# Optimization experiments

Hardware: AMD Instinct MI355X
Metric: run time of the kernel (lower is better)

Reference implementation:

```python
import jax, jax.numpy as jnp
import numpy as np
from jax import lax

DIM = 512
HEADS = 8
B, H, W = 8, 64, 64
EPS = 1e-12  # F.normalize default eps


def pointwise(x, w):
    # 1x1 conv, no bias: [B,C,H,W] x [O,C] -> [B,O,H,W]
    return jnp.einsum('oc,bchw->bohw', w, x)


def depthwise3x3(x, dw):
    # groups=C depthwise 3x3 conv, padding=1, no bias. dw: [C,1,3,3]
    return lax.conv_general_dilated(
        x, dw, window_strides=(1, 1), padding=((1, 1), (1, 1)),
        feature_group_count=x.shape[1],
        dimension_numbers=('NCHW', 'OIHW', 'NCHW'))


def setup_inputs() -> dict:
    key = jax.random.key(0)
    ks = jax.random.split(key, 8)
    s = 1.0 / np.sqrt(DIM)
    return {
        'x': jax.random.normal(ks[0], (B, DIM, H, W), jnp.float32),
        'w_q': jax.random.normal(ks[1], (DIM, DIM), jnp.float32) * s,
        'w_k': jax.random.normal(ks[2], (DIM, DIM), jnp.float32) * s,
        'w_v': jax.random.normal(ks[3], (DIM, DIM), jnp.float32) * s,
        'dw_q': jax.random.normal(ks[4], (DIM, 1, 3, 3), jnp.float32) * (1.0 / 3.0),
        'dw_k': jax.random.normal(ks[5], (DIM, 1, 3, 3), jnp.float32) * (1.0 / 3.0),
        'dw_v': jax.random.normal(ks[6], (DIM, 1, 3, 3), jnp.float32) * (1.0 / 3.0),
        'w_proj': jax.random.normal(ks[7], (DIM, DIM), jnp.float32) * s,
        'temperature': jnp.ones((HEADS, 1, 1), jnp.float32),
    }


def reference(x, w_q, w_k, w_v, dw_q, dw_k, dw_v, w_proj, temperature):
    b, c, h, w = x.shape
    d = c // HEADS
    hw = h * w

    q = depthwise3x3(pointwise(x, w_q), dw_q)
    k = depthwise3x3(pointwise(x, w_k), dw_k)
    v = depthwise3x3(pointwise(x, w_v), dw_v)

    # b (h d) x y -> b h d (x y)
    q = q.reshape(b, HEADS, d, hw)
    k = k.reshape(b, HEADS, d, hw)
    v = v.reshape(b, HEADS, d, hw)

    # L2-normalize over spatial axis (F.normalize, eps=1e-12)
    q = q / jnp.maximum(jnp.linalg.norm(q, axis=-1, keepdims=True), EPS)
    k = k / jnp.maximum(jnp.linalg.norm(k, axis=-1, keepdims=True), EPS)

    # channel attention: [b,h,d,d]
    attn = jnp.einsum('bhdn,bhen->bhde', q, k) * temperature
    attn = jax.nn.softmax(attn, axis=-1)
    out = jnp.einsum('bhde,bhen->bhdn', attn, v)  # [b,h,d,hw]

    out = out.reshape(b, c, h, w)
    return pointwise(out, w_proj)
```

## Files before the change

### kernel.cpp

```cpp
#include <hip/hip_runtime.h>
#include <hip/hip_bf16.h>
#include <stdint.h>

#define DEV __device__ __forceinline__

typedef __attribute__((ext_vector_type(8))) short   s16x8;
typedef __attribute__((ext_vector_type(8))) __bf16  bf16x8;
typedef __attribute__((ext_vector_type(4))) float   f32x4;

static constexpr int BATCH = 8;
static constexpr int DIM   = 512;
static constexpr int HEADS = 8;
static constexpr int HD    = 64;
static constexpr int HW    = 4096;
static constexpr int CQKV  = 1536;
static constexpr int NSPLIT = 8;

DEV void gload16(const void* g, void* l) {
  __builtin_amdgcn_global_load_lds(
      (const __attribute__((address_space(1))) void*)g,
      (__attribute__((address_space(3))) void*)l,
      16, 0, 0);
}

DEV f32x4 mfma16x32(s16x8 a, s16x8 b, f32x4 c) {
  return __builtin_amdgcn_mfma_f32_16x16x32_bf16(
      __builtin_bit_cast(bf16x8, a), __builtin_bit_cast(bf16x8, b), c, 0, 0, 0);
}

DEV float b2f(short x) {
  unsigned u = (unsigned)(unsigned short)x << 16;
  return __uint_as_float(u);
}
DEV short f2b(float f) { return __builtin_bit_cast(short, __float2bfloat16(f)); }

__global__ __launch_bounds__(256) void trx_prep(
    const float* __restrict__ x, __hip_bfloat16* __restrict__ XT,
    const float* __restrict__ wq, const float* __restrict__ wk,
    const float* __restrict__ wv, const float* __restrict__ wp,
    __hip_bfloat16* __restrict__ wqkv, __hip_bfloat16* __restrict__ wpb)
{
  const int t = threadIdx.x;
  if (blockIdx.z == 8) {
    long i0 = (((long)blockIdx.y * 64 + blockIdx.x) * 256 + t) * 8;
    const float* src;
    __hip_bfloat16* dst;
    long off;
    if (i0 < (long)CQKV * DIM) {
      int r = (int)(i0 >> 9);
      src = (r < 512) ? wq : (r < 1024) ? wk : wv;
      off = (long)(r & 511) * DIM + (i0 & 511);
      dst = wqkv + i0;
    } else {
      long j0 = i0 - (long)CQKV * DIM;
      src = wp; off = j0; dst = wpb + j0;
    }
    float4 a = *(const float4*)&src[off];
    float4 b = *(const float4*)&src[off + 4];
    s16x8 v;
    v[0] = f2b(a.x); v[1] = f2b(a.y); v[2] = f2b(a.z); v[3] = f2b(a.w);
    v[4] = f2b(b.x); v[5] = f2b(b.y); v[6] = f2b(b.z); v[7] = f2b(b.w);
    *(s16x8*)dst = v;
    return;
  }
  __shared__ float tile[64 * 65];
  const int n0 = blockIdx.x * 64, c0 = blockIdx.y * 64, b = blockIdx.z;
#pragma unroll
  for (int i = 0; i < 16; ++i) {
    int f = i * 256 + t; int ci = f >> 6, nj = f & 63;
    tile[ci * 65 + nj] = x[((long)b * DIM + c0 + ci) * HW + n0 + nj];
  }
  __syncthreads();
#pragma unroll
  for (int i = 0; i < 16; ++i) {
    int f = i * 256 + t; int ni = f >> 6, cj = f & 63;
    XT[((long)b * HW + n0 + ni) * DIM + c0 + cj] = __float2bfloat16(tile[cj * 65 + ni]);
  }
}

__global__ __launch_bounds__(512) void gemm_bt2(
    const __hip_bfloat16* __restrict__ A,
    const __hip_bfloat16* __restrict__ Bt,
    __hip_bfloat16* __restrict__ Cout,
    int M, int N, int K, long bt_bstride, long c_bstride)
{
  __shared__ __hip_bfloat16 lds[32768];
  const int t = threadIdx.x, w = t >> 6, l = t & 63;
  const int wm = w >> 2, wn = w & 3;
  const int m0 = blockIdx.y * 256, n0 = blockIdx.x * 256, b = blockIdx.z;
  const __hip_bfloat16* Bb = Bt + (long)b * bt_bstride;
  __hip_bfloat16* ldsA = lds;
  __hip_bfloat16* ldsB = lds + 16384;

  const int fr = l & 15, g = l >> 4;
  f32x4 acc[8][4] = {};

  for (int k0 = 0; k0 < K; k0 += 64) {
#pragma unroll
    for (int q = 0; q < 4; ++q) {
      int id = q * 512 + t;
      int r = id >> 3;
      int c = (id & 7) ^ (r & 7);
      gload16(A  + (long)(m0 + r) * K + k0 + c * 8, &ldsA[id * 8]);
      gload16(Bb + (long)(n0 + r) * K + k0 + c * 8, &ldsB[id * 8]);
    }
    __syncthreads();
#pragma unroll
    for (int kk = 0; kk < 64; kk += 32) {
      s16x8 af[8], bfr[4];
#pragma unroll
      for (int mi = 0; mi < 8; ++mi) {
        int ar = wm * 128 + mi * 16 + fr;
        int col = (kk + g * 8) ^ ((ar & 7) << 3);
        af[mi] = *(const s16x8*)&ldsA[ar * 64 + col];
      }
#pragma unroll
      for (int ni = 0; ni < 4; ++ni) {
        int br = wn * 64 + ni * 16 + fr;
        int col = (kk + g * 8) ^ ((br & 7) << 3);
        bfr[ni] = *(const s16x8*)&ldsB[br * 64 + col];
      }
#pragma unroll
      for (int mi = 0; mi < 8; ++mi)
#pragma unroll
        for (int ni = 0; ni < 4; ++ni)
          acc[mi][ni] = mfma16x32(af[mi], bfr[ni], acc[mi][ni]);
    }
    __syncthreads();
  }

  const int row0 = m0 + wm * 128, col0 = n0 + wn * 64;
#pragma unroll
  for (int mi = 0; mi < 8; ++mi)
#pragma unroll
    for (int ni = 0; ni < 4; ++ni)
#pragma unroll
      for (int j = 0; j < 4; ++j) {
        long rr = row0 + mi * 16 + (l >> 4) * 4 + j;
        long cc = col0 + ni * 16 + fr;
        Cout[(long)b * c_bstride + rr * N + cc] = __float2bfloat16(acc[mi][ni][j]);
      }
}

template <bool OUT_BF16>
__global__ __launch_bounds__(512, 2) void gemm_bt8(
    const __hip_bfloat16* __restrict__ A,
    const __hip_bfloat16* __restrict__ Bt,
    void* __restrict__ Cout,
    int M, int N, int K, long bt_bstride, long c_bstride)
{
  __shared__ __hip_bfloat16 lds[65536];
  const int t = threadIdx.x, w = t >> 6, l = t & 63;
  const int wm = w >> 2, wn = w & 3;
  const int m0 = blockIdx.y * 256, n0 = blockIdx.x * 256, b = blockIdx.z;
  const __hip_bfloat16* Bb = Bt + (long)b * bt_bstride;

  const int rl = t >> 3;
  const int ch = ((t & 7) ^ (rl & 7)) * 8;
  const int fr = l & 15, fk = (l >> 4) * 8;
  const int fswz = (l & 7) << 3;

  auto stageA = [&](int p, int h, int u) {
    const __hip_bfloat16* src = A + (long)(m0 + h * 64 + rl) * K + u * 64 + ch;
    __hip_bfloat16* dst = lds + p * 16384 + h * 8192 + w * 512;
    gload16(src, dst);
    gload16(src + 128l * K, dst + 4096);
  };
  auto stageB = [&](int p, int hb, int u) {
    const __hip_bfloat16* src = Bb + (long)(n0 + hb * 128 + rl) * K + u * 64 + ch;
    __hip_bfloat16* dst = lds + 32768 + p * 16384 + hb * 8192 + w * 512;
    gload16(src, dst);
    gload16(src + 64l * K, dst + 4096);
  };

  f32x4 acc[8][4] = {};
  const int NT = K >> 6;

  stageB(0, 0, 0); stageB(0, 1, 0); stageA(0, 0, 0); stageA(0, 1, 0);
  stageB(1, 0, 1); stageB(1, 1, 1); stageA(1, 0, 1);
  asm volatile("s_waitcnt vmcnt(6)" ::: "memory");
  __builtin_amdgcn_s_barrier();

  for (int u = 0; u < NT; ++u) {
    const int p = u & 1;
    const __hip_bfloat16* lA = lds + p * 16384 + wm * 4096;
    const __hip_bfloat16* lB = lds + 32768 + p * 16384 + (wn >> 1) * 8192
                             + (wn & 1) * 4096;
    s16x8 bfr[2][4];
#pragma unroll
    for (int q = 0; q < 4; ++q) {
      s16x8 afr[2][2];
#pragma unroll
      for (int kk = 0; kk < 2; ++kk)
#pragma unroll
        for (int mi = 0; mi < 2; ++mi)
          afr[kk][mi] = *(const s16x8*)&lA[(q >> 1) * 8192
              + ((q & 1) * 32 + mi * 16 + fr) * 64 + ((kk * 32 + fk) ^ fswz)];
      if (q == 0) {
#pragma unroll
        for (int kk = 0; kk < 2; ++kk)
#pragma unroll
          for (int ni = 0; ni < 4; ++ni)
            bfr[kk][ni] = *(const s16x8*)&lB[(ni * 16 + fr) * 64
                + ((kk * 32 + fk) ^ fswz)];
      }
      if (q == 0)      { if (u + 1 < NT) stageA(p ^ 1, 1, u + 1); }
      else if (q == 1) { if (u + 2 < NT) stageB(p, 0, u + 2); }
      else if (q == 2) { if (u + 2 < NT) stageB(p, 1, u + 2); }
      else {
        if (u + 2 < NT) stageA(p, 0, u + 2);
        if (u == NT - 2) asm volatile("s_waitcnt vmcnt(0)" ::: "memory");
        else             asm volatile("s_waitcnt vmcnt(6)" ::: "memory");
      }
      __builtin_amdgcn_s_barrier();
      asm volatile("s_waitcnt lgkmcnt(0)" ::: "memory");
      __builtin_amdgcn_sched_barrier(0);
      __builtin_amdgcn_s_setprio(1);
#pragma unroll
      for (int kk = 0; kk < 2; ++kk)
#pragma unroll
        for (int mi = 0; mi < 2; ++mi)
#pragma unroll
          for (int ni = 0; ni < 4; ++ni)
            acc[q * 2 + mi][ni] = mfma16x32(afr[kk][mi], bfr[kk][ni],
                                            acc[q * 2 + mi][ni]);
      __builtin_amdgcn_s_setprio(0);
      __builtin_amdgcn_s_barrier();
    }
  }

  const int row0 = m0 + wm * 128, col0 = n0 + wn * 64;
#pragma unroll
  for (int mi = 0; mi < 8; ++mi)
#pragma unroll
    for (int ni = 0; ni < 4; ++ni)
#pragma unroll
      for (int j = 0; j < 4; ++j) {
        long rr = row0 + mi * 16 + (l >> 4) * 4 + j;
        long cc = col0 + ni * 16 + fr;
        float v = acc[mi][ni][j];
        if (OUT_BF16)
          ((__hip_bfloat16*)Cout)[(long)b * c_bstride + rr * N + cc] = __float2bfloat16(v);
        else
          ((float*)Cout)[(long)b * c_bstride + rr * N + cc] = v;
      }
}

__global__ __launch_bounds__(256) void dwconv(
    __hip_bfloat16* __restrict__ P,
    const float* __restrict__ dwq, const float* __restrict__ dwk,
    const float* __restrict__ dwv, float* __restrict__ rnorm)
{
  __shared__ float pl[66 * 67];
  __shared__ float red4[4];
  const int c = blockIdx.x, b = blockIdx.y, t = threadIdx.x;
  const int w = t >> 6, l = t & 63;

  if (t < 66) { pl[t] = 0.f; pl[65 * 67 + t] = 0.f; }
  if (t >= 128 && t < 192) { pl[(t - 127) * 67] = 0.f; }
  if (t >= 192)            { pl[(t - 191) * 67 + 65] = 0.f; }

  const long base = ((long)b * CQKV + c) * HW;
  const int y = t >> 2, x0 = (t & 3) * 16;
  s16x8 v0 = *(const s16x8*)&P[base + t * 16];
  s16x8 v1 = *(const s16x8*)&P[base + t * 16 + 8];
#pragma unroll
  for (int j = 0; j < 8; ++j) {
    pl[(y + 1) * 67 + x0 + 1 + j] = b2f(v0[j]);
    pl[(y + 1) * 67 + x0 + 9 + j] = b2f(v1[j]);
  }
  __syncthreads();

  const int qkv = c >> 9, cc = c & 511;
  const float* dw = ((qkv == 0) ? dwq : (qkv == 1) ? dwk : dwv) + (long)cc * 9;
  const float w0 = dw[0], w1 = dw[1], w2 = dw[2], w3 = dw[3], w4 = dw[4],
              w5 = dw[5], w6 = dw[6], w7 = dw[7], w8 = dw[8];

  const float* r0 = &pl[y * 67 + x0];
  float outv[16];
  float ss = 0.f;
#pragma unroll
  for (int j = 0; j < 16; ++j) {
    float s = w0 * r0[j]       + w1 * r0[j + 1]   + w2 * r0[j + 2]
            + w3 * r0[j + 67]  + w4 * r0[j + 68]  + w5 * r0[j + 69]
            + w6 * r0[j + 134] + w7 * r0[j + 135] + w8 * r0[j + 136];
    outv[j] = s;
    ss += s * s;
  }
  s16x8 o0, o1;
#pragma unroll
  for (int j = 0; j < 8; ++j) { o0[j] = f2b(outv[j]); o1[j] = f2b(outv[j + 8]); }
  *(s16x8*)&P[base + t * 16]     = o0;
  *(s16x8*)&P[base + t * 16 + 8] = o1;

  if (qkv < 2) {
#pragma unroll
    for (int off = 32; off; off >>= 1) ss += __shfl_down(ss, off);
    if (l == 0) red4[w] = ss;
    __syncthreads();
    if (t == 0)
      rnorm[(long)b * 1024 + qkv * 512 + cc] =
          1.f / fmaxf(sqrtf(red4[0] + red4[1] + red4[2] + red4[3]), 1e-12f);
  }
}

__global__ __launch_bounds__(256) void transpose_v(
    const __hip_bfloat16* __restrict__ P, __hip_bfloat16* __restrict__ VT)
{
  __shared__ __hip_bfloat16 tile[64 * 65];
  const int n0 = blockIdx.x * 64, h = blockIdx.y, b = blockIdx.z;
  const int t = threadIdx.x;
#pragma unroll
  for (int i = 0; i < 16; ++i) {
    int f = i * 256 + t; int ei = f >> 6, nj = f & 63;
    tile[ei * 65 + nj] = P[((long)b * CQKV + 1024 + h * HD + ei) * HW + n0 + nj];
  }
  __syncthreads();
#pragma unroll
  for (int i = 0; i < 16; ++i) {
    int f = i * 256 + t; int ni = f >> 6, ej = f & 63;
    VT[(((long)b * HEADS + h) * HW + n0 + ni) * HD + ej] = tile[ej * 65 + ni];
  }
}

__global__ __launch_bounds__(256) void attn_partial(__hip_bfloat16* __restrict__ P)
{
  __shared__ __hip_bfloat16 ldsQ[64 * 128];
  __shared__ __hip_bfloat16 ldsK[64 * 128];
  const int t = threadIdx.x, w = t >> 6, l = t & 63;
  const int sp = blockIdx.x, h = blockIdx.y, b = blockIdx.z;
  const int wr = w >> 1, wc = w & 1;

  const long qbase = ((long)b * CQKV + h * HD) * HW;
  const long kbase = ((long)b * CQKV + 512 + h * HD) * HW;

  f32x4 acc[2][2] = {};

  const int kend = sp * 512 + 512;
  for (int k0 = sp * 512; k0 < kend; k0 += 128) {
#pragma unroll
    for (int i = 0; i < 4; ++i) {
      int r = w * 16 + i * 4 + (l >> 4);
      int c = (l & 15) ^ (r & 7);
      gload16(P + qbase + (long)r * HW + k0 + c * 8, &ldsQ[w * 2048 + i * 512]);
      gload16(P + kbase + (long)r * HW + k0 + c * 8, &ldsK[w * 2048 + i * 512]);
    }
    __syncthreads();
#pragma unroll
    for (int kk = 0; kk < 128; kk += 32) {
      s16x8 af[2], bfr[2];
#pragma unroll
      for (int mi = 0; mi < 2; ++mi) {
        int ar = wr * 32 + mi * 16 + (l & 15);
        int col = (kk + (l >> 4) * 8) ^ ((ar & 7) << 3);
        af[mi] = *(const s16x8*)&ldsQ[ar * 128 + col];
      }
#pragma unroll
      for (int ni = 0; ni < 2; ++ni) {
        int br = wc * 32 + ni * 16 + (l & 15);
        int col = (kk + (l >> 4) * 8) ^ ((br & 7) << 3);
        bfr[ni] = *(const s16x8*)&ldsK[br * 128 + col];
      }
#pragma unroll
      for (int mi = 0; mi < 2; ++mi)
#pragma unroll
        for (int ni = 0; ni < 2; ++ni)
          acc[mi][ni] = mfma16x32(af[mi], bfr[ni], acc[mi][ni]);
    }
    __syncthreads();
  }

  float* part = (float*)((char*)P + (long)b * (CQKV * HW * 2) + (1024l * HW * 2))
              + ((long)h * NSPLIT + sp) * 4096;
#pragma unroll
  for (int mi = 0; mi < 2; ++mi)
#pragma unroll
    for (int ni = 0; ni < 2; ++ni)
#pragma unroll
      for (int j = 0; j < 4; ++j) {
        int row = wr * 32 + mi * 16 + (l >> 4) * 4 + j;
        int col = wc * 32 + ni * 16 + (l & 15);
        part[row * 64 + col] = acc[mi][ni][j];
      }
}

__global__ __launch_bounds__(256) void attn_softmax(
    const __hip_bfloat16* __restrict__ P, const float* __restrict__ rnorm,
    const float* __restrict__ temp, __hip_bfloat16* __restrict__ attnb)
{
  __shared__ float S[64 * 65];
  const int t = threadIdx.x, h = blockIdx.x, b = blockIdx.y;
  const float* part = (const float*)((const char*)P + (long)b * (CQKV * HW * 2)
                                     + (1024l * HW * 2))
                    + (long)h * NSPLIT * 4096;
  const float tm = temp[h];

  for (int i = t; i < 4096; i += 256) {
    float s = 0.f;
#pragma unroll
    for (int p = 0; p < NSPLIT; ++p) s += part[p * 4096 + i];
    int r = i >> 6, c = i & 63;
    float rq = rnorm[(long)b * 1024 + h * HD + r];
    float rk = rnorm[(long)b * 1024 + 512 + h * HD + c];
    S[r * 65 + c] = s * rq * rk * tm;
  }
  __syncthreads();

  if (t < 64) {
    float m = -3.4e38f;
    for (int e = 0; e < 64; ++e) m = fmaxf(m, S[t * 65 + e]);
    float sum = 0.f;
    for (int e = 0; e < 64; ++e) {
      float ev = __expf(S[t * 65 + e] - m);
      S[t * 65 + e] = ev;
      sum += ev;
    }
    float inv = 1.f / sum;
    for (int e = 0; e < 64; ++e)
      attnb[(((long)b * HEADS + h) * 64 + t) * 64 + e] =
          __float2bfloat16(S[t * 65 + e] * inv);
  }
}

__global__ __launch_bounds__(256) void attn_apply_v(
    const __hip_bfloat16* __restrict__ VT, const __hip_bfloat16* __restrict__ attnb,
    __hip_bfloat16* __restrict__ OT)
{
  __shared__ __hip_bfloat16 ldsV[128 * 64];
  __shared__ __hip_bfloat16 ldsAt[64 * 64];
  const int t = threadIdx.x, w = t >> 6, l = t & 63;
  const int bh = blockIdx.y, b = bh >> 3, h = bh & 7;
  const int n0 = blockIdx.x * 128;

#pragma unroll
  for (int i = 0; i < 4; ++i) {
    int r = w * 32 + i * 8 + (l >> 3);
    int c = (l & 7) ^ (r & 7);
    gload16(VT + ((long)bh * HW + n0 + r) * HD + c * 8, &ldsV[w * 2048 + i * 512]);
  }
#pragma unroll
  for (int i = 0; i < 2; ++i) {
    int r = w * 16 + i * 8 + (l >> 3);
    int c = (l & 7) ^ (r & 7);
    gload16(attnb + ((long)bh * 64 + r) * 64 + c * 8, &ldsAt[w * 1024 + i * 512]);
  }
  __syncthreads();

  f32x4 acc[2][4] = {};
#pragma unroll
  for (int kk = 0; kk < 64; kk += 32) {
    s16x8 af[2], bfr[4];
#pragma unroll
    for (int mi = 0; mi < 2; ++mi) {
      int ar = w * 32 + mi * 16 + (l & 15);
      int col = (kk + (l >> 4) * 8) ^ ((ar & 7) << 3);
      af[mi] = *(const s16x8*)&ldsV[ar * 64 + col];
    }
#pragma unroll
    for (int ni = 0; ni < 4; ++ni) {
      int br = ni * 16 + (l & 15);
      int col = (kk + (l >> 4) * 8) ^ ((br & 7) << 3);
      bfr[ni] = *(const s16x8*)&ldsAt[br * 64 + col];
    }
#pragma unroll
    for (int mi = 0; mi < 2; ++mi)
#pragma unroll
      for (int ni = 0; ni < 4; ++ni)
        acc[mi][ni] = mfma16x32(af[mi], bfr[ni], acc[mi][ni]);
  }

#pragma unroll
  for (int mi = 0; mi < 2; ++mi)
#pragma unroll
    for (int ni = 0; ni < 4; ++ni)
#pragma unroll
      for (int j = 0; j < 4; ++j) {
        long n = n0 + w * 32 + mi * 16 + (l >> 4) * 4 + j;
        long c = h * HD + ni * 16 + (l & 15);
        OT[((long)b * HW + n) * DIM + c] = __float2bfloat16(acc[mi][ni][j]);
      }
}

extern "C" void kernel_launch(void* const* d_in, const int* in_sizes, int n_in,
                              void* d_out, int out_size, void* d_ws, size_t ws_size,
                              hipStream_t stream)
{
  const float* x    = (const float*)d_in[0];
  const float* wq   = (const float*)d_in[1];
  const float* wk   = (const float*)d_in[2];
  const float* wv   = (const float*)d_in[3];
  const float* dwq  = (const float*)d_in[4];
  const float* dwk  = (const float*)d_in[5];
  const float* dwv  = (const float*)d_in[6];
  const float* wp   = (const float*)d_in[7];
  const float* temp = (const float*)d_in[8];
  float* out = (float*)d_out;

  char* ws = (char*)d_ws;
  __hip_bfloat16* wqkv  = (__hip_bfloat16*)(ws + 0);
  __hip_bfloat16* wpb   = (__hip_bfloat16*)(ws + 1572864);
  float*          rnorm = (float*)(ws + 2097152);
  __hip_bfloat16* attnb = (__hip_bfloat16*)(ws + 2129920);
  __hip_bfloat16* XT    = (__hip_bfloat16*)(ws + (4l << 20));
  __hip_bfloat16* VT    = XT;
  __hip_bfloat16* P     = (__hip_bfloat16*)(ws + (40l << 20));
  __hip_bfloat16* OT    = P;

  trx_prep<<<dim3(64, 8, 9), 256, 0, stream>>>(x, XT, wq, wk, wv, wp, wqkv, wpb);
  gemm_bt2<<<dim3(16, 6, 8), 512, 0, stream>>>(
      wqkv, XT, P, CQKV, HW, DIM, (long)HW * DIM, (long)CQKV * HW);
  dwconv<<<dim3(1536, 8), 256, 0, stream>>>(P, dwq, dwk, dwv, rnorm);
  transpose_v<<<dim3(64, 8, 8), 256, 0, stream>>>(P, VT);
  attn_partial<<<dim3(NSPLIT, 8, 8), 256, 0, stream>>>(P);
  attn_softmax<<<dim3(8, 8), 256, 0, stream>>>(P, rnorm, temp, attnb);
  attn_apply_v<<<dim3(32, 64), 256, 0, stream>>>(VT, attnb, OT);
  gemm_bt8<false><<<dim3(16, 2, 8), 512, 0, stream>>>(
      wpb, OT, out, DIM, HW, DIM, (long)HW * DIM, (long)DIM * HW);
}
```

Measured before the change: 192.7 us.

## Shrink QKV GEMM tiles to 128x128 and add XCD-aware block swizzle

The QKV projection GEMM moves from 256x256 tiles with 512 threads to 128x128 tiles with 256 threads, which raises the workgroup count from 768 to 3072 for better occupancy and load balance across CUs. Both GEMMs now launch a 1D grid and remap block IDs with a swizzle that groups consecutive tiles onto the same XCD. The goal is better L2 reuse of the weight and activation tiles. The smaller tiles lower per-block data reuse and raise global/LDS traffic per FLOP. The bf16-output template of gemm_bt8 is also removed.

Result: slower. 196.6 us (+2.0%).

```diff
diff --git a/kernel.cpp b/kernel.cpp
--- a/kernel.cpp
+++ b/kernel.cpp
@@ -78,50 +78,54 @@
   }
 }
 
-__global__ __launch_bounds__(512) void gemm_bt2(
+__global__ __launch_bounds__(256) void gemm_bt(
     const __hip_bfloat16* __restrict__ A,
     const __hip_bfloat16* __restrict__ Bt,
     __hip_bfloat16* __restrict__ Cout,
-    int M, int N, int K, long bt_bstride, long c_bstride)
-{
-  __shared__ __hip_bfloat16 lds[32768];
+    int NXT, int MT, int K, int nwg,
+    int N, long bt_bstride, long c_bstride)
+{
+  const int lid = blockIdx.x;
+  const int swz = (lid & 7) * (nwg >> 3) + (lid >> 3);
+  const int nx = swz % NXT;
+  const int my = (swz / NXT) % MT;
+  const int b  = swz / (NXT * MT);
+
+  __shared__ __hip_bfloat16 ldsA[128 * 64];
+  __shared__ __hip_bfloat16 ldsB[128 * 64];
   const int t = threadIdx.x, w = t >> 6, l = t & 63;
-  const int wm = w >> 2, wn = w & 3;
-  const int m0 = blockIdx.y * 256, n0 = blockIdx.x * 256, b = blockIdx.z;
+  const int m0 = my * 128, n0 = nx * 128;
+  const int wr = w >> 1, wc = w & 1;
   const __hip_bfloat16* Bb = Bt + (long)b * bt_bstride;
-  __hip_bfloat16* ldsA = lds;
-  __hip_bfloat16* ldsB = lds + 16384;
-
-  const int fr = l & 15, g = l >> 4;
-  f32x4 acc[8][4] = {};
+
+  f32x4 acc[4][4] = {};
 
   for (int k0 = 0; k0 < K; k0 += 64) {
 #pragma unroll
-    for (int q = 0; q < 4; ++q) {
-      int id = q * 512 + t;
-      int r = id >> 3;
-      int c = (id & 7) ^ (r & 7);
-      gload16(A  + (long)(m0 + r) * K + k0 + c * 8, &ldsA[id * 8]);
-      gload16(Bb + (long)(n0 + r) * K + k0 + c * 8, &ldsB[id * 8]);
+    for (int i = 0; i < 4; ++i) {
+      int r = w * 32 + i * 8 + (l >> 3);
+      int c = (l & 7) ^ (r & 7);
+      gload16(A  + (long)(m0 + r) * K + k0 + c * 8, &ldsA[w * 2048 + i * 512]);
+      gload16(Bb + (long)(n0 + r) * K + k0 + c * 8, &ldsB[w * 2048 + i * 512]);
     }
     __syncthreads();
 #pragma unroll
     for (int kk = 0; kk < 64; kk += 32) {
-      s16x8 af[8], bfr[4];
-#pragma unroll
-      for (int mi = 0; mi < 8; ++mi) {
-        int ar = wm * 128 + mi * 16 + fr;
-        int col = (kk + g * 8) ^ ((ar & 7) << 3);
+      s16x8 af[4], bfr[4];
+#pragma unroll
+      for (int mi = 0; mi < 4; ++mi) {
+        int ar = wr * 64 + mi * 16 + (l & 15);
+        int col = (kk + (l >> 4) * 8) ^ ((ar & 7) << 3);
         af[mi] = *(const s16x8*)&ldsA[ar * 64 + col];
       }
 #pragma unroll
       for (int ni = 0; ni < 4; ++ni) {
-        int br = wn * 64 + ni * 16 + fr;
-        int col = (kk + g * 8) ^ ((br & 7) << 3);
+        int br = wc * 64 + ni * 16 + (l & 15);
+        int col = (kk + (l >> 4) * 8) ^ ((br & 7) << 3);
         bfr[ni] = *(const s16x8*)&ldsB[br * 64 + col];
       }
 #pragma unroll
-      for (int mi = 0; mi < 8; ++mi)
+      for (int mi = 0; mi < 4; ++mi)
 #pragma unroll
         for (int ni = 0; ni < 4; ++ni)
           acc[mi][ni] = mfma16x32(af[mi], bfr[ni], acc[mi][ni]);
@@ -129,30 +133,36 @@
     __syncthreads();
   }
 
-  const int row0 = m0 + wm * 128, col0 = n0 + wn * 64;
-#pragma unroll
-  for (int mi = 0; mi < 8; ++mi)
+  const int row0 = m0 + wr * 64, col0 = n0 + wc * 64;
+#pragma unroll
+  for (int mi = 0; mi < 4; ++mi)
 #pragma unroll
     for (int ni = 0; ni < 4; ++ni)
 #pragma unroll
       for (int j = 0; j < 4; ++j) {
         long rr = row0 + mi * 16 + (l >> 4) * 4 + j;
-        long cc = col0 + ni * 16 + fr;
+        long cc = col0 + ni * 16 + (l & 15);
         Cout[(long)b * c_bstride + rr * N + cc] = __float2bfloat16(acc[mi][ni][j]);
       }
 }
 
-template <bool OUT_BF16>
 __global__ __launch_bounds__(512, 2) void gemm_bt8(
     const __hip_bfloat16* __restrict__ A,
     const __hip_bfloat16* __restrict__ Bt,
-    void* __restrict__ Cout,
-    int M, int N, int K, long bt_bstride, long c_bstride)
-{
+    float* __restrict__ Cout,
+    int NXT, int MT, int K, int nwg,
+    int N, long bt_bstride, long c_bstride)
+{
+  const int lid = blockIdx.x;
+  const int swz = (lid & 7) * (nwg >> 3) + (lid >> 3);
+  const int nx = swz % NXT;
+  const int my = (swz / NXT) % MT;
+  const int b  = swz / (NXT * MT);
+
   __shared__ __hip_bfloat16 lds[65536];
   const int t = threadIdx.x, w = t >> 6, l = t & 63;
   const int wm = w >> 2, wn = w & 3;
-  const int m0 = blockIdx.y * 256, n0 = blockIdx.x * 256, b = blockIdx.z;
+  const int m0 = my * 256, n0 = nx * 256;
   const __hip_bfloat16* Bb = Bt + (long)b * bt_bstride;
 
   const int rl = t >> 3;
@@ -238,11 +248,7 @@
       for (int j = 0; j < 4; ++j) {
         long rr = row0 + mi * 16 + (l >> 4) * 4 + j;
         long cc = col0 + ni * 16 + fr;
-        float v = acc[mi][ni][j];
-        if (OUT_BF16)
-          ((__hip_bfloat16*)Cout)[(long)b * c_bstride + rr * N + cc] = __float2bfloat16(v);
-        else
-          ((float*)Cout)[(long)b * c_bstride + rr * N + cc] = v;
+        Cout[(long)b * c_bstride + rr * N + cc] = acc[mi][ni][j];
       }
 }
 
@@ -507,13 +513,13 @@
   __hip_bfloat16* OT    = P;
 
   trx_prep<<<dim3(64, 8, 9), 256, 0, stream>>>(x, XT, wq, wk, wv, wp, wqkv, wpb);
-  gemm_bt2<<<dim3(16, 6, 8), 512, 0, stream>>>(
-      wqkv, XT, P, CQKV, HW, DIM, (long)HW * DIM, (long)CQKV * HW);
+  gemm_bt<<<3072, 256, 0, stream>>>(
+      wqkv, XT, P, 32, 12, DIM, 3072, HW, (long)HW * DIM, (long)CQKV * HW);
   dwconv<<<dim3(1536, 8), 256, 0, stream>>>(P, dwq, dwk, dwv, rnorm);
   transpose_v<<<dim3(64, 8, 8), 256, 0, stream>>>(P, VT);
   attn_partial<<<dim3(NSPLIT, 8, 8), 256, 0, stream>>>(P);
   attn_softmax<<<dim3(8, 8), 256, 0, stream>>>(P, rnorm, temp, attnb);
   attn_apply_v<<<dim3(32, 64), 256, 0, stream>>>(VT, attnb, OT);
-  gemm_bt8<false><<<dim3(16, 2, 8), 512, 0, stream>>>(
-      wpb, OT, out, DIM, HW, DIM, (long)HW * DIM, (long)DIM * HW);
-}
+  gemm_bt8<<<256, 512, 0, stream>>>(
+      wpb, OT, out, 16, 2, DIM, 256, HW, (long)HW * DIM, (long)DIM * HW);
+}
```
